# Optimization experiments

Measured on AMD Instinct MI355X. Metric: run time of the kernel, lower is better.

Reference implementation:

```python
import jax, jax.numpy as jnp
import numpy as np

EMBED_DIM = 1024
NUM_HEADS = 16
HEAD_DIM = EMBED_DIM // NUM_HEADS


def setup_inputs() -> dict:
    key = jax.random.key(0)
    ks = jax.random.split(key, 11)
    L, N, E = 2048, 2, EMBED_DIM
    S = 2048
    def xavier(k, shape):
        fan_in, fan_out = shape[1], shape[0]
        limit = float(np.sqrt(6.0 / (fan_in + fan_out)))
        return jax.random.uniform(k, shape, jnp.float32, -limit, limit)
    return {
        "query": jax.random.normal(ks[0], (L, N, E), jnp.float32),
        "key": jax.random.normal(ks[1], (S, N, E), jnp.float32),
        "value": jax.random.normal(ks[2], (S, N, E), jnp.float32),
        "Wq": xavier(ks[3], (E, E)), "bq": jnp.zeros((E,), jnp.float32),
        "Wk": xavier(ks[4], (E, E)), "bk": jnp.zeros((E,), jnp.float32),
        "Wv": xavier(ks[5], (E, E)), "bv": jnp.zeros((E,), jnp.float32),
        "Wo": xavier(ks[6], (E, E)), "bo": jnp.zeros((E,), jnp.float32),
    }


def reference(query, key, value, Wq, bq, Wk, bk, Wv, bv, Wo, bo):
    # query/key/value: [L, N, E] (seq-first, batch_first=False)
    L, N, E = query.shape
    S = key.shape[0]
    H, D = NUM_HEADS, HEAD_DIM
    q = query @ Wq.T + bq   # [L, N, E]
    k = key @ Wk.T + bk     # [S, N, E]
    v = value @ Wv.T + bv   # [S, N, E]
    # [L, N*H, D] -> [N*H, L, D]
    q = q.reshape(L, N * H, D).transpose(1, 0, 2)
    k = k.reshape(S, N * H, D).transpose(1, 0, 2)
    v = v.reshape(S, N * H, D).transpose(1, 0, 2)
    scores = jnp.einsum("bld,bsd->bls", q, k) / jnp.sqrt(jnp.float32(D))  # [N*H, L, S]
    attn = jax.nn.softmax(scores, axis=-1)  # dropout p=0.0 -> identity
    out = jnp.einsum("bls,bsd->bld", attn, v)  # [N*H, L, D]
    out = out.transpose(1, 0, 2).reshape(L, N, E)
    attn_output = out @ Wo.T + bo  # [L, N, E]
    # need_weights=True, average_attn_weights=True
    attn_weights = attn.reshape(N, H, L, S).mean(axis=1)  # [N, L, S]
    return attn_output, attn_weights
```

## Files before the change

kernel.cpp:

```cpp
#include <hip/hip_runtime.h>

#define EDIM 1024
#define LSEQ 2048
#define NBATCH 2
#define NHEADS 16
#define HDIM 64
#define QSCALE 0.18033688011112042f

typedef unsigned short us;
typedef __attribute__((ext_vector_type(8))) short short8;
typedef __attribute__((ext_vector_type(4))) float floatx4;
typedef __attribute__((ext_vector_type(16))) float floatx16;

#define MFMA16(a, b, c) __builtin_amdgcn_mfma_f32_16x16x32_bf16((a), (b), (c), 0, 0, 0)
#define MFMA32(a, b, c) __builtin_amdgcn_mfma_f32_32x32x16_bf16((a), (b), (c), 0, 0, 0)
#define ZERO16 ((floatx16){0.f,0.f,0.f,0.f,0.f,0.f,0.f,0.f,0.f,0.f,0.f,0.f,0.f,0.f,0.f,0.f})

#define WAIT_VM8 asm volatile("s_waitcnt vmcnt(8)" ::: "memory")
#define WAIT_VM4 asm volatile("s_waitcnt vmcnt(4)" ::: "memory")
#define WAIT_VM0 asm volatile("s_waitcnt vmcnt(0)" ::: "memory")
#define WAIT_LGKM0 asm volatile("s_waitcnt lgkmcnt(0)" ::: "memory")
#define CFENCE asm volatile("" ::: "memory")

__device__ __forceinline__ us f2bf(float f) {
  unsigned int u = __float_as_uint(f);
  u += 0x7fffu + ((u >> 16) & 1u);
  return (us)(u >> 16);
}

__device__ __forceinline__ void gload16(const void* g, void* l) {
  __builtin_amdgcn_global_load_lds((const __attribute__((address_space(1))) unsigned int*)g,
                                   (__attribute__((address_space(3))) unsigned int*)l, 16, 0, 0);
}

__device__ __forceinline__ unsigned int cvtpk(float lo, float hi_) {
  unsigned int r;
  asm("v_cvt_pk_bf16_f32 %0, %1, %2" : "=v"(r) : "v"(lo), "v"(hi_));
  return r;
}
__device__ __forceinline__ void plswap(unsigned int& a, unsigned int& b) {
  asm("v_permlane32_swap_b32 %0, %1" : "+v"(a), "+v"(b));
}
__device__ __forceinline__ short8 mkfrag(unsigned int a, unsigned int b, unsigned int c,
                                         unsigned int d) {
  union { unsigned int u[4]; short8 v; } x;
  x.u[0] = a; x.u[1] = b; x.u[2] = c; x.u[3] = d;
  return x.v;
}
__device__ __forceinline__ void pack2(const floatx16 p, short8& f0, short8& f1) {
  unsigned int A = cvtpk(p[0], p[1]), B = cvtpk(p[4], p[5]); plswap(A, B);
  unsigned int C = cvtpk(p[2], p[3]), D = cvtpk(p[6], p[7]); plswap(C, D);
  f0 = mkfrag(A, C, B, D);
  unsigned int E = cvtpk(p[8], p[9]), F = cvtpk(p[12], p[13]); plswap(E, F);
  unsigned int G = cvtpk(p[10], p[11]), H = cvtpk(p[14], p[15]); plswap(G, H);
  f1 = mkfrag(E, G, F, H);
}

__device__ __forceinline__ short8 onesfrag() {
  union { us u[8]; short8 v; } x;
#pragma unroll
  for (int i = 0; i < 8; ++i) x.u[i] = 0x3F80;
  return x.v;
}

__global__ void k_f2bf_all(const float* q, const float* k, const float* v,
                           const float* wq, const float* wk, const float* wv, const float* wo,
                           us* dq, us* dk, us* dv, us* dwq, us* dwk, us* dwv, us* dwo) {
  const int z = blockIdx.y;
  const float* s; us* d; int n8;
  if (z == 0)      { s = q;  d = dq;  n8 = 524288; }
  else if (z == 1) { s = k;  d = dk;  n8 = 524288; }
  else if (z == 2) { s = v;  d = dv;  n8 = 524288; }
  else if (z == 3) { s = wq; d = dwq; n8 = 131072; }
  else if (z == 4) { s = wk; d = dwk; n8 = 131072; }
  else if (z == 5) { s = wv; d = dwv; n8 = 131072; }
  else             { s = wo; d = dwo; n8 = 131072; }
  int i = blockIdx.x * blockDim.x + threadIdx.x;
  int stride = gridDim.x * blockDim.x;
  for (; i < n8; i += stride) {
    float4 a = ((const float4*)s)[2 * i];
    float4 b = ((const float4*)s)[2 * i + 1];
    union { us u[8]; uint4 vv; } o;
    o.u[0] = f2bf(a.x); o.u[1] = f2bf(a.y); o.u[2] = f2bf(a.z); o.u[3] = f2bf(a.w);
    o.u[4] = f2bf(b.x); o.u[5] = f2bf(b.y); o.u[6] = f2bf(b.z); o.u[7] = f2bf(b.w);
    ((uint4*)d)[i] = o.vv;
  }
}

template <int MODE>
__device__ __forceinline__ void gemm_core(us* pool,
                                          const us* __restrict__ A, const us* __restrict__ B,
                                          const float* __restrict__ bias, void* __restrict__ outp,
                                          int row0, int col0, float scale) {
  us* const Asb[2] = {pool, pool + 8192};
  us* const Bsb[2] = {pool + 4096, pool + 12288};
  const int t = threadIdx.x;
  const int w = t >> 6, lane = t & 63;
  const int g = lane >> 4, lr = lane & 15;
  const int wm = (w & 1) * 64, wn = (w >> 1) * 64;
  const int srow = lane >> 2, scol = (lane & 3) * 8;
  const int cA = 2 * w;
  const us* Asrc = A + (size_t)(row0 + cA * 16 + srow) * EDIM + scol;
  const us* Bsrc = B + (size_t)(col0 + cA * 16 + srow) * EDIM + scol;

  floatx4 acc[4][4];
#pragma unroll
  for (int mi = 0; mi < 4; ++mi)
#pragma unroll
    for (int ni = 0; ni < 4; ++ni) acc[mi][ni] = (floatx4){0.f, 0.f, 0.f, 0.f};

  auto stage = [&](int kt, int b) {
    const int k0 = kt * 32;
    gload16(Asrc + k0, Asb[b] + cA * 512);
    gload16(Asrc + 16 * EDIM + k0, Asb[b] + cA * 512 + 512);
    gload16(Bsrc + k0, Bsb[b] + cA * 512);
    gload16(Bsrc + 16 * EDIM + k0, Bsb[b] + cA * 512 + 512);
  };

  stage(0, 0);
  stage(1, 1);

  for (int kt = 0; kt < 32; ++kt) {
    if (kt < 31) { WAIT_VM4; } else { WAIT_VM0; }
    __builtin_amdgcn_s_barrier();
    CFENCE;
    const us* Ac = Asb[kt & 1];
    const us* Bc = Bsb[kt & 1];
    short8 af[4], bfr[4];
#pragma unroll
    for (int mi = 0; mi < 4; ++mi) af[mi] = *(const short8*)&Ac[(wm + mi * 16 + lr) * 32 + g * 8];
#pragma unroll
    for (int ni = 0; ni < 4; ++ni) bfr[ni] = *(const short8*)&Bc[(wn + ni * 16 + lr) * 32 + g * 8];
#pragma unroll
    for (int mi = 0; mi < 4; ++mi)
#pragma unroll
      for (int ni = 0; ni < 4; ++ni) acc[mi][ni] = MFMA16(af[mi], bfr[ni], acc[mi][ni]);
    WAIT_LGKM0;
    __builtin_amdgcn_s_barrier();
    CFENCE;
    if (kt + 2 < 32) stage(kt + 2, kt & 1);
  }

  if (MODE == 1) {
    us* Ct = pool;
#pragma unroll
    for (int ni = 0; ni < 4; ++ni) {
      const int colloc = wn + ni * 16 + lr;
      const float bv = bias[col0 + colloc];
#pragma unroll
      for (int mi = 0; mi < 4; ++mi) {
        const int b = wm + mi * 16 + 4 * g;
        unsigned int lo = (unsigned int)f2bf(acc[mi][ni][0] + bv) |
                          ((unsigned int)f2bf(acc[mi][ni][2] + bv) << 16);
        unsigned int hi = (unsigned int)f2bf(acc[mi][ni][1] + bv) |
                          ((unsigned int)f2bf(acc[mi][ni][3] + bv) << 16);
        *(unsigned int*)&Ct[colloc * 136 + (b >> 1)] = lo;
        *(unsigned int*)&Ct[colloc * 136 + 64 + (b >> 1)] = hi;
      }
    }
    __syncthreads();
    const int rr = t >> 1, half = t & 1;
    const int c = col0 + rr, h = c >> 6, d = c & 63;
    us* dst = (us*)outp + (((size_t)half * NHEADS + h) * HDIM + d) * LSEQ + (row0 >> 1);
    const us* srcRow = &Ct[rr * 136 + half * 64];
#pragma unroll
    for (int j = 0; j < 8; ++j)
      *(uint4*)(dst + j * 8) = *(const uint4*)(srcRow + j * 8);
  } else {
#pragma unroll
    for (int ni = 0; ni < 4; ++ni) {
      const int col = col0 + wn + ni * 16 + lr;
      const float bv = bias[col];
#pragma unroll
      for (int mi = 0; mi < 4; ++mi) {
#pragma unroll
        for (int i = 0; i < 4; ++i) {
          const int row = row0 + wm + mi * 16 + g * 4 + i;
          const float v = (acc[mi][ni][i] + bv) * scale;
          if (MODE == 2) {
            ((float*)outp)[(size_t)row * EDIM + col] = v;
          } else {
            const int n = row & 1, sq = row >> 1;
            const int h = col >> 6, d = col & 63;
            ((us*)outp)[(((size_t)n * NHEADS + h) * LSEQ + sq) * HDIM + d] = f2bf(v);
          }
        }
      }
    }
  }
}

__global__ __launch_bounds__(256) void k_gemm_qkv(
    const us* __restrict__ Xq, const us* __restrict__ Xk, const us* __restrict__ Xv,
    const us* __restrict__ Wqb, const us* __restrict__ Wkb, const us* __restrict__ Wvb,
    const float* __restrict__ bq, const float* __restrict__ bk, const float* __restrict__ bv,
    us* __restrict__ qo, us* __restrict__ ko, us* __restrict__ vo) {
  __shared__ us pool[17408];
  const int z = blockIdx.z;
  if (z == 0)      gemm_core<0>(pool, Xq, Wqb, bq, qo, blockIdx.x * 128, blockIdx.y * 128, QSCALE);
  else if (z == 1) gemm_core<0>(pool, Xk, Wkb, bk, ko, blockIdx.x * 128, blockIdx.y * 128, 1.0f);
  else             gemm_core<1>(pool, Xv, Wvb, bv, vo, blockIdx.x * 128, blockIdx.y * 128, 1.0f);
}

__global__ __launch_bounds__(256) void k_gemm_o(const us* __restrict__ A, const us* __restrict__ B,
                                                const float* __restrict__ bias, float* __restrict__ out) {
  __shared__ us pool[16384];
  gemm_core<2>(pool, A, B, bias, out, blockIdx.x * 128, blockIdx.y * 128, 1.0f);
}

__global__ __launch_bounds__(128) void k_attn(const us* __restrict__ qb, const us* __restrict__ kb,
                                              const us* __restrict__ vt, float* __restrict__ rell,
                                              us* __restrict__ O) {
  __shared__ us Ks[2][4096];
  __shared__ us Vs[2][4096];
  const int bh = blockIdx.x;
  const int l0 = blockIdx.y * 64;
  const int t = threadIdx.x, w = t >> 6, lane = t & 63;
  const int ql = lane & 31, hi = lane >> 5;
  const int lbase = l0 + w * 32;

  short8 qf[4];
  {
    const us* qptr = qb + ((size_t)bh * LSEQ + lbase + ql) * HDIM + hi * 8;
#pragma unroll
    for (int dt = 0; dt < 4; ++dt) qf[dt] = *(const short8*)(qptr + dt * 16);
  }

  int off0[4], off1[4];
#pragma unroll
  for (int j = 0; j < 4; ++j) {
    off0[j] = ql * 64 + (((2 * j + hi) ^ (ql & 7)) << 3);
    off1[j] = (32 + ql) * 64 + (((2 * j + hi) ^ (ql & 7)) << 3);
  }

  const int srA = lane >> 3;
  const int scA = ((lane & 7) ^ (lane >> 3)) * 8;
  const us* Kbase = kb + (size_t)bh * LSEQ * HDIM;
  const us* Vbase = vt + (size_t)bh * HDIM * LSEQ;
  const us* Ksrc[4];
  const us* Vsrc[4];
#pragma unroll
  for (int i = 0; i < 4; ++i) {
    const int jj = 4 * w + i;
    Ksrc[i] = Kbase + (jj * 8 + srA) * HDIM + scA;
    Vsrc[i] = Vbase + (size_t)(jj * 8 + srA) * LSEQ + scA;
  }

  floatx16 oacc0 = ZERO16, oacc1 = ZERO16, ellmf = ZERO16;
  const short8 onesf = onesfrag();

  auto stageKV = [&](int kt, int b) {
    const int so = kt * 64;
#pragma unroll
    for (int i = 0; i < 4; ++i) {
      gload16(Ksrc[i] + so * HDIM, &Ks[b][(4 * w + i) * 512]);
      gload16(Vsrc[i] + so, &Vs[b][(4 * w + i) * 512]);
    }
  };

  stageKV(0, 0);
  stageKV(1, 1);

  for (int it = 0; it < 32; ++it) {
    if (it < 31) { WAIT_VM8; } else { WAIT_VM0; }
    __builtin_amdgcn_s_barrier();
    CFENCE;
    const us* Kc = Ks[it & 1];
    const us* Vc = Vs[it & 1];

    floatx16 acc0 = ZERO16, acc1 = ZERO16;
    __builtin_amdgcn_s_setprio(1);
#pragma unroll
    for (int dt = 0; dt < 4; ++dt) {
      acc0 = MFMA32(*(const short8*)&Kc[off0[dt]], qf[dt], acc0);
      acc1 = MFMA32(*(const short8*)&Kc[off1[dt]], qf[dt], acc1);
    }
    __builtin_amdgcn_s_setprio(0);
#pragma unroll
    for (int r = 0; r < 16; ++r) {
      acc0[r] = __builtin_amdgcn_exp2f(acc0[r]);
      acc1[r] = __builtin_amdgcn_exp2f(acc1[r]);
    }
    short8 pa0, pa1, pa2, pa3;
    pack2(acc0, pa0, pa1);
    pack2(acc1, pa2, pa3);
    __builtin_amdgcn_s_setprio(1);
#pragma unroll
    for (int dt2 = 0; dt2 < 2; ++dt2) {
      floatx16& oa = dt2 ? oacc1 : oacc0;
      const int* off = dt2 ? off1 : off0;
      oa = MFMA32(pa0, *(const short8*)&Vc[off[0]], oa);
      oa = MFMA32(pa1, *(const short8*)&Vc[off[1]], oa);
      oa = MFMA32(pa2, *(const short8*)&Vc[off[2]], oa);
      oa = MFMA32(pa3, *(const short8*)&Vc[off[3]], oa);
    }
    ellmf = MFMA32(pa0, onesf, ellmf);
    ellmf = MFMA32(pa1, onesf, ellmf);
    ellmf = MFMA32(pa2, onesf, ellmf);
    ellmf = MFMA32(pa3, onesf, ellmf);
    __builtin_amdgcn_s_setprio(0);
    WAIT_LGKM0;
    __builtin_amdgcn_s_barrier();
    CFENCE;
    if (it + 2 < 32) stageKV(it + 2, it & 1);
  }

  float rinv[16];
#pragma unroll
  for (int r = 0; r < 16; ++r) rinv[r] = 1.0f / ellmf[r];
  if (ql == 0) {
#pragma unroll
    for (int r = 0; r < 16; ++r) {
      const int q = (r & 3) + 8 * (r >> 2) + 4 * hi;
      rell[(size_t)bh * LSEQ + lbase + q] = rinv[r];
    }
  }
  const int n = bh >> 4, hh = bh & 15;
  us* obase = O + (size_t)n * EDIM + (size_t)hh * HDIM;
#pragma unroll
  for (int r = 0; r < 16; ++r) {
    const int q = (r & 3) + 8 * (r >> 2) + 4 * hi;
    const size_t l = lbase + q;
    obase[l * (NBATCH * EDIM) + ql] = f2bf(oacc0[r] * rinv[r]);
    obase[l * (NBATCH * EDIM) + 32 + ql] = f2bf(oacc1[r] * rinv[r]);
  }
}

__global__ __launch_bounds__(256, 2) void k_weights(const us* __restrict__ qb, const us* __restrict__ kb,
                                                    const float* __restrict__ rell,
                                                    float* __restrict__ Wout) {
  __shared__ us Ks[2][4096];
  const int l0 = blockIdx.x * 256;
  const int s0 = blockIdx.y * 64;
  const int n = blockIdx.z;
  const int t = threadIdx.x, w = t >> 6, lane = t & 63;
  const int ql = lane & 31, hi = lane >> 5;
  const int lbase = l0 + w * 64;
  const int j0 = 2 * w, j1 = 2 * w + 1;
  const int srA = lane >> 3;
  const int scA = ((lane & 7) ^ (lane >> 3)) * 8;
  const us* Kb0 = kb + ((size_t)(n * NHEADS) * LSEQ + s0 + j0 * 8 + srA) * HDIM + scA;
  const us* Kb1 = kb + ((size_t)(n * NHEADS) * LSEQ + s0 + j1 * 8 + srA) * HDIM + scA;

  int off0[4], off1[4];
#pragma unroll
  for (int j = 0; j < 4; ++j) {
    off0[j] = ql * 64 + (((2 * j + hi) ^ (ql & 7)) << 3);
    off1[j] = (32 + ql) * 64 + (((2 * j + hi) ^ (ql & 7)) << 3);
  }

  floatx16 wa00 = ZERO16, wa01 = ZERO16, wa10 = ZERO16, wa11 = ZERO16;

  gload16(Kb0, &Ks[0][j0 * 512]); gload16(Kb1, &Ks[0][j1 * 512]);

  short8 qc0[4], qc1[4];
  float rlc0, rlc1;
  {
    const us* qp0 = qb + ((size_t)(n * NHEADS) * LSEQ + lbase + ql) * HDIM + hi * 8;
    const us* qp1 = qp0 + 32 * HDIM;
#pragma unroll
    for (int dt = 0; dt < 4; ++dt) {
      qc0[dt] = *(const short8*)(qp0 + dt * 16);
      qc1[dt] = *(const short8*)(qp1 + dt * 16);
    }
    rlc0 = rell[(size_t)(n * NHEADS) * LSEQ + lbase + ql];
    rlc1 = rell[(size_t)(n * NHEADS) * LSEQ + lbase + 32 + ql];
  }
  __syncthreads();

  for (int h = 0; h < NHEADS; ++h) {
    const int cur = h & 1;
    short8 qn0[4], qn1[4];
    float rln0 = 0.f, rln1 = 0.f;
    if (h < NHEADS - 1) {
      us* Kn2 = Ks[cur ^ 1];
      gload16(Kb0 + (size_t)(h + 1) * LSEQ * HDIM, Kn2 + j0 * 512);
      gload16(Kb1 + (size_t)(h + 1) * LSEQ * HDIM, Kn2 + j1 * 512);
      const us* qp0 = qb + ((size_t)(n * NHEADS + h + 1) * LSEQ + lbase + ql) * HDIM + hi * 8;
      const us* qp1 = qp0 + 32 * HDIM;
#pragma unroll
      for (int dt = 0; dt < 4; ++dt) {
        qn0[dt] = *(const short8*)(qp0 + dt * 16);
        qn1[dt] = *(const short8*)(qp1 + dt * 16);
      }
      rln0 = rell[(size_t)(n * NHEADS + h + 1) * LSEQ + lbase + ql];
      rln1 = rell[(size_t)(n * NHEADS + h + 1) * LSEQ + lbase + 32 + ql];
    }
    const us* Kc = Ks[cur];
    short8 kf0[4], kf1[4];
#pragma unroll
    for (int dt = 0; dt < 4; ++dt) {
      kf0[dt] = *(const short8*)&Kc[off0[dt]];
      kf1[dt] = *(const short8*)&Kc[off1[dt]];
    }
    {
      floatx16 aA = ZERO16, aB = ZERO16;
#pragma unroll
      for (int dt = 0; dt < 4; ++dt) {
        aA = MFMA32(kf0[dt], qc0[dt], aA);
        aB = MFMA32(kf1[dt], qc0[dt], aB);
      }
#pragma unroll
      for (int r = 0; r < 16; ++r) {
        wa00[r] += __builtin_amdgcn_exp2f(aA[r]) * rlc0;
        wa01[r] += __builtin_amdgcn_exp2f(aB[r]) * rlc0;
      }
    }
    {
      floatx16 cA = ZERO16, cB = ZERO16;
#pragma unroll
      for (int dt = 0; dt < 4; ++dt) {
        cA = MFMA32(kf0[dt], qc1[dt], cA);
        cB = MFMA32(kf1[dt], qc1[dt], cB);
      }
#pragma unroll
      for (int r = 0; r < 16; ++r) {
        wa10[r] += __builtin_amdgcn_exp2f(cA[r]) * rlc1;
        wa11[r] += __builtin_amdgcn_exp2f(cB[r]) * rlc1;
      }
    }
#pragma unroll
    for (int dt = 0; dt < 4; ++dt) { qc0[dt] = qn0[dt]; qc1[dt] = qn1[dt]; }
    rlc0 = rln0; rlc1 = rln1;
    __syncthreads();
  }

  float* wb0 = Wout + (size_t)n * LSEQ * LSEQ + (size_t)(lbase + ql) * LSEQ + s0;
  float* wb1 = Wout + (size_t)n * LSEQ * LSEQ + (size_t)(lbase + 32 + ql) * LSEQ + s0;
#pragma unroll
  for (int r = 0; r < 16; ++r) {
    const int cr = (r & 3) + 8 * (r >> 2) + 4 * hi;
    wb0[cr] = wa00[r] * 0.0625f;
    wb0[32 + cr] = wa01[r] * 0.0625f;
    wb1[cr] = wa10[r] * 0.0625f;
    wb1[32 + cr] = wa11[r] * 0.0625f;
  }
}

extern "C" void kernel_launch(void* const* d_in, const int* in_sizes, int n_in,
                              void* d_out, int out_size, void* d_ws, size_t ws_size,
                              hipStream_t stream) {
  const float* query = (const float*)d_in[0];
  const float* key   = (const float*)d_in[1];
  const float* value = (const float*)d_in[2];
  const float* Wq = (const float*)d_in[3]; const float* bq = (const float*)d_in[4];
  const float* Wk = (const float*)d_in[5]; const float* bk = (const float*)d_in[6];
  const float* Wv = (const float*)d_in[7]; const float* bv = (const float*)d_in[8];
  const float* Wo = (const float*)d_in[9]; const float* bo = (const float*)d_in[10];

  const size_t MB = 1u << 20;
  char* ws = (char*)d_ws;
  us* Xq  = (us*)(ws + 0 * MB);
  us* Xk  = (us*)(ws + 8 * MB);
  us* Xv  = (us*)(ws + 16 * MB);
  us* Wqb = (us*)(ws + 24 * MB);
  us* Wkb = (us*)(ws + 26 * MB);
  us* Wvb = (us*)(ws + 28 * MB);
  us* Wob = (us*)(ws + 30 * MB);
  us* qbuf = (us*)(ws + 32 * MB);
  us* kbuf = (us*)(ws + 40 * MB);
  us* Vt   = (us*)(ws + 48 * MB);
  us* Obuf = (us*)(ws + 56 * MB);
  float* rell = (float*)(ws + 64 * MB);

  k_f2bf_all<<<dim3(256, 7), 256, 0, stream>>>(query, key, value, Wq, Wk, Wv, Wo,
                                               Xq, Xk, Xv, Wqb, Wkb, Wvb, Wob);

  k_gemm_qkv<<<dim3(32, 8, 3), 256, 0, stream>>>(Xq, Xk, Xv, Wqb, Wkb, Wvb, bq, bk, bv,
                                                 qbuf, kbuf, Vt);

  k_attn<<<dim3(32, 32), 128, 0, stream>>>(qbuf, kbuf, Vt, rell, Obuf);

  k_gemm_o<<<dim3(32, 8), 256, 0, stream>>>(Obuf, Wob, bo, (float*)d_out);
  k_weights<<<dim3(8, 32, 2), 256, 0, stream>>>(qbuf, kbuf, rell, (float*)d_out + 4194304);
}
```

Before: 164.4 us.

## Use 4-wave attention blocks with 4-slot KV ring and single barrier

The attention kernel moves from 2 to 4 waves per block, each block covering 128 queries, so every K/V tile staged in LDS is shared by twice as many query rows. The double buffer becomes a 4-slot ring, and the prefetch for tile it+2 is issued right after the top barrier. This removes the second per-iteration barrier and the lgkm wait. The cost is LDS use rising from 32KB to 64KB per block and half as many blocks in the grid.

```diff
diff --git a/kernel.cpp b/kernel.cpp
--- a/kernel.cpp
+++ b/kernel.cpp
@@ -16,7 +16,6 @@
 #define MFMA32(a, b, c) __builtin_amdgcn_mfma_f32_32x32x16_bf16((a), (b), (c), 0, 0, 0)
 #define ZERO16 ((floatx16){0.f,0.f,0.f,0.f,0.f,0.f,0.f,0.f,0.f,0.f,0.f,0.f,0.f,0.f,0.f,0.f})
 
-#define WAIT_VM8 asm volatile("s_waitcnt vmcnt(8)" ::: "memory")
 #define WAIT_VM4 asm volatile("s_waitcnt vmcnt(4)" ::: "memory")
 #define WAIT_VM0 asm volatile("s_waitcnt vmcnt(0)" ::: "memory")
 #define WAIT_LGKM0 asm volatile("s_waitcnt lgkmcnt(0)" ::: "memory")
@@ -208,13 +207,13 @@
   gemm_core<2>(pool, A, B, bias, out, blockIdx.x * 128, blockIdx.y * 128, 1.0f);
 }
 
-__global__ __launch_bounds__(128) void k_attn(const us* __restrict__ qb, const us* __restrict__ kb,
+__global__ __launch_bounds__(256) void k_attn(const us* __restrict__ qb, const us* __restrict__ kb,
                                               const us* __restrict__ vt, float* __restrict__ rell,
                                               us* __restrict__ O) {
-  __shared__ us Ks[2][4096];
-  __shared__ us Vs[2][4096];
+  __shared__ us Ks[4][4096];
+  __shared__ us Vs[4][4096];
   const int bh = blockIdx.x;
-  const int l0 = blockIdx.y * 64;
+  const int l0 = blockIdx.y * 128;
   const int t = threadIdx.x, w = t >> 6, lane = t & 63;
   const int ql = lane & 31, hi = lane >> 5;
   const int lbase = l0 + w * 32;
@@ -233,40 +232,37 @@
     off1[j] = (32 + ql) * 64 + (((2 * j + hi) ^ (ql & 7)) << 3);
   }
 
+  const int j0 = 2 * w, j1 = 2 * w + 1;
   const int srA = lane >> 3;
   const int scA = ((lane & 7) ^ (lane >> 3)) * 8;
   const us* Kbase = kb + (size_t)bh * LSEQ * HDIM;
   const us* Vbase = vt + (size_t)bh * HDIM * LSEQ;
-  const us* Ksrc[4];
-  const us* Vsrc[4];
-#pragma unroll
-  for (int i = 0; i < 4; ++i) {
-    const int jj = 4 * w + i;
-    Ksrc[i] = Kbase + (jj * 8 + srA) * HDIM + scA;
-    Vsrc[i] = Vbase + (size_t)(jj * 8 + srA) * LSEQ + scA;
-  }
+  const us* Ksrc0 = Kbase + (j0 * 8 + srA) * HDIM + scA;
+  const us* Ksrc1 = Kbase + (j1 * 8 + srA) * HDIM + scA;
+  const us* Vsrc0 = Vbase + (size_t)(j0 * 8 + srA) * LSEQ + scA;
+  const us* Vsrc1 = Vbase + (size_t)(j1 * 8 + srA) * LSEQ + scA;
 
   floatx16 oacc0 = ZERO16, oacc1 = ZERO16, ellmf = ZERO16;
   const short8 onesf = onesfrag();
 
   auto stageKV = [&](int kt, int b) {
     const int so = kt * 64;
-#pragma unroll
-    for (int i = 0; i < 4; ++i) {
-      gload16(Ksrc[i] + so * HDIM, &Ks[b][(4 * w + i) * 512]);
-      gload16(Vsrc[i] + so, &Vs[b][(4 * w + i) * 512]);
-    }
+    gload16(Ksrc0 + so * HDIM, &Ks[b][j0 * 512]);
+    gload16(Ksrc1 + so * HDIM, &Ks[b][j1 * 512]);
+    gload16(Vsrc0 + so, &Vs[b][j0 * 512]);
+    gload16(Vsrc1 + so, &Vs[b][j1 * 512]);
   };
 
   stageKV(0, 0);
   stageKV(1, 1);
 
   for (int it = 0; it < 32; ++it) {
-    if (it < 31) { WAIT_VM8; } else { WAIT_VM0; }
+    if (it < 31) { WAIT_VM4; } else { WAIT_VM0; }
     __builtin_amdgcn_s_barrier();
     CFENCE;
-    const us* Kc = Ks[it & 1];
-    const us* Vc = Vs[it & 1];
+    if (it + 2 < 32) stageKV(it + 2, (it + 2) & 3);
+    const us* Kc = Ks[it & 3];
+    const us* Vc = Vs[it & 3];
 
     floatx16 acc0 = ZERO16, acc1 = ZERO16;
     __builtin_amdgcn_s_setprio(1);
@@ -299,10 +295,6 @@
     ellmf = MFMA32(pa2, onesf, ellmf);
     ellmf = MFMA32(pa3, onesf, ellmf);
     __builtin_amdgcn_s_setprio(0);
-    WAIT_LGKM0;
-    __builtin_amdgcn_s_barrier();
-    CFENCE;
-    if (it + 2 < 32) stageKV(it + 2, it & 1);
   }
 
   float rinv[16];
@@ -469,7 +461,7 @@
   k_gemm_qkv<<<dim3(32, 8, 3), 256, 0, stream>>>(Xq, Xk, Xv, Wqb, Wkb, Wvb, bq, bk, bv,
                                                  qbuf, kbuf, Vt);
 
-  k_attn<<<dim3(32, 32), 128, 0, stream>>>(qbuf, kbuf, Vt, rell, Obuf);
+  k_attn<<<dim3(32, 16), 256, 0, stream>>>(qbuf, kbuf, Vt, rell, Obuf);
 
   k_gemm_o<<<dim3(32, 8), 256, 0, stream>>>(Obuf, Wob, bo, (float*)d_out);
   k_weights<<<dim3(8, 32, 2), 256, 0, stream>>>(qbuf, kbuf, rell, (float*)d_out + 4194304);
```

Measured after the change: 156.4 us. 1.05x faster.
